# Kernel optimization log

Hardware: AMD Instinct MI355X
Metric: run time of the kernel (lower is better)

Reference implementation:

```python
import jax, jax.numpy as jnp
import numpy as np

B, J, F_IN, F_OUT = 16384, 17, 128, 128

def setup_inputs() -> dict:
    key = jax.random.key(0)
    k1, k2, k3, k4 = jax.random.split(key, 4)
    # xavier-ish scales
    x = jax.random.normal(k1, (B, J, F_IN), dtype=jnp.float32)
    W = jax.random.normal(k2, (2, F_IN, F_OUT), dtype=jnp.float32) * (1.414 * (6.0 / (F_IN + F_OUT)) ** 0.5 / 3.0)
    M = jax.random.normal(k3, (J, F_OUT), dtype=jnp.float32) * 0.5
    adj = jnp.eye(J, dtype=jnp.float32)          # adj == None path: learnable identity
    adj2 = jnp.full((J, J), 1e-6, dtype=jnp.float32)
    stdv = 1.0 / (F_OUT ** 0.5)
    bias = jax.random.uniform(k4, (F_OUT,), dtype=jnp.float32, minval=-stdv, maxval=stdv)
    return {"x": x, "W": W, "M": M, "adj": adj, "adj2": adj2, "bias": bias}

def reference(x, W, M, adj, adj2, bias):
    # h0, h1: [B, J, F_OUT]
    h0 = jnp.einsum('bjf,fg->bjg', x, W[0])
    h1 = jnp.einsum('bjf,fg->bjg', x, W[1])
    A = adj + adj2
    A = (A.T + A) * 0.5                      # symmetrize, [J, J]
    E = jnp.eye(A.shape[0], dtype=x.dtype)
    A_diag = A * E                           # self connections
    A_off = A * (1.0 - E)                    # neighbor connections
    # modulated aggregation: [J,J] x [B,J,F] -> [B,J,F]
    out = (jnp.einsum('ij,bjg->big', A_diag, M * h0)
           + jnp.einsum('ij,bjg->big', A_off, M * h1))
    return out + bias[None, None, :]
```

## Files before the change

kernel.cpp:

```cpp
#include <hip/hip_runtime.h>

#define J 17
#define F 128
#define TB 16
#define THREADS 512

typedef __attribute__((ext_vector_type(4))) float f32x4;
typedef __attribute__((ext_vector_type(8))) short bf16x8;

__device__ __forceinline__ unsigned short f2bf(float f) {
    unsigned u = __builtin_bit_cast(unsigned, f);
    u += 0x7fffu + ((u >> 16) & 1u);
    return (unsigned short)(u >> 16);
}

__device__ __forceinline__ f32x4 fma4(float a, f32x4 v, f32x4 c) {
#pragma unroll
    for (int r = 0; r < 4; ++r) c[r] = __builtin_fmaf(a, v[r], c[r]);
    return c;
}

__global__ void prep(const float* __restrict__ W, const float* __restrict__ adj,
                     const float* __restrict__ adj2, float* __restrict__ wsA,
                     unsigned short* __restrict__ WT) {
    int t = blockIdx.x * 256 + threadIdx.x;
    for (int idx = t; idx < 2 * F * F; idx += 16 * 256) {
        int mat = idx >> 14;
        int rem = idx & 16383;
        int g = rem >> 7, k = rem & 127;
        WT[idx] = f2bf(W[mat * 16384 + k * F + g]);
    }
    if (blockIdx.x == 0) {
        for (int idx = threadIdx.x; idx < J * J; idx += 256) {
            int i = idx / J, j = idx % J;
            float a = 0.5f * (adj[i*J+j] + adj2[i*J+j] + adj[j*J+i] + adj2[j*J+i]);
            wsA[idx] = (i == j) ? 0.0f : a;
            if (i == j) wsA[J * J + i] = a;
        }
    }
}

__global__ __launch_bounds__(THREADS, 2) void mgcn_kernel(
    const float* __restrict__ x, const float* __restrict__ Mw,
    const float* __restrict__ bias, const float* __restrict__ wsA,
    const unsigned short* __restrict__ WT, float* __restrict__ out) {

    __shared__ __align__(16) unsigned char xs[TB * J * F * 2];
    __shared__ __align__(16) float Ms[J * F];

    const int tid = threadIdx.x;
    const int b0  = blockIdx.x * TB;

    for (int idx = tid; idx < J * F / 4; idx += THREADS)
        ((float4*)Ms)[idx] = ((const float4*)Mw)[idx];

    const float4* xg = (const float4*)(x + (size_t)b0 * (J * F));
#pragma unroll
    for (int it = 0; it < (TB * J * F / 4) / THREADS; ++it) {
        int fi = it * THREADS + tid;
        float4 v = xg[fi];
        int b  = fi / (J * F / 4);
        int r  = fi - b * (J * F / 4);
        int j  = r >> 5;
        int k0 = (r & 31) * 4;
        unsigned byte = (unsigned)(b * (J * F * 2) + j * (F * 2) + k0 * 2);
        byte ^= (unsigned)((b & 7) << 4);
        ushort4 u;
        u.x = f2bf(v.x); u.y = f2bf(v.y); u.z = f2bf(v.z); u.w = f2bf(v.w);
        *(ushort4*)(xs + byte) = u;
    }

    const int wave = tid >> 6;
    const int lane = tid & 63;
    const int lrow = lane & 15;
    const int lq   = lane >> 4;
    const int grow = wave * 16 + lrow;
    const int gq   = wave * 16 + lq * 4;

    const f32x4 bias4 = *(const f32x4*)(bias + gq);
    f32x4 acc[J];
#pragma unroll
    for (int i = 0; i < J; ++i) acc[i] = bias4;

    const float* __restrict__ Aoff  = wsA;
    const float* __restrict__ Adiag = wsA + J * J;
    const unsigned rbase = (unsigned)(lrow * (J * F * 2));
    const unsigned swz   = (unsigned)((lrow & 7) << 4);

    __syncthreads();

    {
        bf16x8 wf0[4];
#pragma unroll
        for (int ks = 0; ks < 4; ++ks)
            wf0[ks] = __builtin_bit_cast(bf16x8,
                *(const uint4*)(WT + (size_t)grow * F + ks * 32 + lq * 8));
#pragma unroll
        for (int j = 0; j < J; ++j) {
            f32x4 h0 = {0.f, 0.f, 0.f, 0.f};
#pragma unroll
            for (int ks = 0; ks < 4; ++ks) {
                unsigned byte = (rbase + (unsigned)(j * (F * 2) + ks * 64 + lq * 16)) ^ swz;
                bf16x8 xf = __builtin_bit_cast(bf16x8, *(const uint4*)(xs + byte));
                h0 = __builtin_amdgcn_mfma_f32_16x16x32_bf16(wf0[ks], xf, h0, 0, 0, 0);
            }
            f32x4 mj = *(const f32x4*)&Ms[j * F + gq];
            f32x4 t0;
#pragma unroll
            for (int r = 0; r < 4; ++r) t0[r] = mj[r] * h0[r];
            acc[j] = fma4(Adiag[j], t0, acc[j]);
        }
    }

    {
        bf16x8 wf1[4];
#pragma unroll
        for (int ks = 0; ks < 4; ++ks)
            wf1[ks] = __builtin_bit_cast(bf16x8,
                *(const uint4*)(WT + (size_t)(F * F) + (size_t)grow * F + ks * 32 + lq * 8));
#pragma unroll
        for (int j = 0; j < J; ++j) {
            f32x4 h1 = {0.f, 0.f, 0.f, 0.f};
#pragma unroll
            for (int ks = 0; ks < 4; ++ks) {
                unsigned byte = (rbase + (unsigned)(j * (F * 2) + ks * 64 + lq * 16)) ^ swz;
                bf16x8 xf = __builtin_bit_cast(bf16x8, *(const uint4*)(xs + byte));
                h1 = __builtin_amdgcn_mfma_f32_16x16x32_bf16(wf1[ks], xf, h1, 0, 0, 0);
            }
            f32x4 mj = *(const f32x4*)&Ms[j * F + gq];
            f32x4 mh1;
#pragma unroll
            for (int r = 0; r < 4; ++r) mh1[r] = mj[r] * h1[r];
#pragma unroll
            for (int i = 0; i < J; ++i)
                acc[i] = fma4(Aoff[i * J + j], mh1, acc[i]);
        }
    }

#pragma unroll 1
    for (int r = 0; r < 2; ++r) {
        __syncthreads();
        if ((lrow >> 3) == r) {
            const int bl = lrow & 7;
            const unsigned base = (unsigned)(bl * (J * F * 4) + gq * 4);
            const unsigned esw  = (unsigned)((bl & 3) << 5);
#pragma unroll
            for (int i = 0; i < J; ++i)
                *(f32x4*)(xs + ((base + (unsigned)(i * F * 4)) ^ esw)) = acc[i];
        }
        __syncthreads();
        const size_t gbase = ((size_t)b0 + r * 8) * (J * F);
        for (int f = tid; f < 8 * J * F / 4; f += THREADS) {
            unsigned byte = (unsigned)f * 16u;
            unsigned bl   = byte / (unsigned)(J * F * 4);
            float4 v = *(const float4*)(xs + (byte ^ ((bl & 3) << 5)));
            *(float4*)(out + gbase + (size_t)f * 4) = v;
        }
    }
}

extern "C" void kernel_launch(void* const* d_in, const int* in_sizes, int n_in,
                              void* d_out, int out_size, void* d_ws, size_t ws_size,
                              hipStream_t stream) {
    const float* x    = (const float*)d_in[0];
    const float* W    = (const float*)d_in[1];
    const float* Mw   = (const float*)d_in[2];
    const float* adj  = (const float*)d_in[3];
    const float* adj2 = (const float*)d_in[4];
    const float* bias = (const float*)d_in[5];
    float* out = (float*)d_out;
    float* wsA = (float*)d_ws;
    unsigned short* WT = (unsigned short*)((char*)d_ws + 2048);

    int Btot = in_sizes[0] / (J * F);
    prep<<<16, 256, 0, stream>>>(W, adj, adj2, wsA, WT);
    mgcn_kernel<<<Btot / TB, THREADS, 0, stream>>>(x, Mw, bias, wsA, WT, out);
}
```

Measured before the change: 86.86 us.

## Stage x in two joint chunks and bf16 output staging to cut LDS

Splits the joint dimension into two chunks of 9 and 8 joints. Each chunk is loaded, converted to bf16 and processed in turn, so the shared x buffer holds only 9 joints per batch row. Output accumulators are now staged through shared memory as bf16 instead of fp32 so they fit the smaller buffer. The goal is a much smaller LDS footprint per block so more blocks can be resident per CU and hide memory latency. The costs are an extra barrier per chunk and bf16 rounding of the final output, which loses precision.

```diff
diff --git a/kernel.cpp b/kernel.cpp
--- a/kernel.cpp
+++ b/kernel.cpp
@@ -4,6 +4,7 @@
 #define F 128
 #define TB 16
 #define THREADS 512
+#define JSTRIDE 9
 
 typedef __attribute__((ext_vector_type(4))) float f32x4;
 typedef __attribute__((ext_vector_type(8))) short bf16x8;
@@ -13,11 +14,13 @@
     u += 0x7fffu + ((u >> 16) & 1u);
     return (unsigned short)(u >> 16);
 }
+__device__ __forceinline__ float bf2f(unsigned short s) {
+    return __builtin_bit_cast(float, (unsigned)s << 16);
+}
 
 __device__ __forceinline__ f32x4 fma4(float a, f32x4 v, f32x4 c) {
-#pragma unroll
-    for (int r = 0; r < 4; ++r) c[r] = __builtin_fmaf(a, v[r], c[r]);
-    return c;
+    f32x4 av = {a, a, a, a};
+    return __builtin_elementwise_fma(av, v, c);
 }
 
 __global__ void prep(const float* __restrict__ W, const float* __restrict__ adj,
@@ -40,12 +43,87 @@
     }
 }
 
+template<int JC, int J0>
+__device__ __forceinline__ void chunk(
+    const float* __restrict__ x, unsigned char* xs, const float* Ms,
+    const float* __restrict__ Aoff, const float* __restrict__ Adiag,
+    const unsigned short* __restrict__ WT, f32x4* acc,
+    int tid, int b0, int lrow, int lq, int grow, int gq) {
+
+#pragma unroll
+    for (int it = 0; it < JC; ++it) {
+        int fi = it * THREADS + tid;
+        int b  = fi / (JC * 32);
+        int r  = fi - b * (JC * 32);
+        int jj = r >> 5;
+        int k4 = r & 31;
+        const float4 v = *(const float4*)(x + (size_t)(b0 + b) * (J * F)
+                                            + (J0 + jj) * F + k4 * 4);
+        unsigned byte = (unsigned)(((b * JSTRIDE + jj) << 8) + (k4 << 3));
+        byte ^= (unsigned)((b & 7) << 4);
+        ushort4 u;
+        u.x = f2bf(v.x); u.y = f2bf(v.y); u.z = f2bf(v.z); u.w = f2bf(v.w);
+        *(ushort4*)(xs + byte) = u;
+    }
+    __syncthreads();
+
+    const unsigned rbase = (unsigned)(lrow * (JSTRIDE * 256));
+    const unsigned swz   = (unsigned)((lrow & 7) << 4);
+
+    {
+        bf16x8 wf[4];
+#pragma unroll
+        for (int ks = 0; ks < 4; ++ks)
+            wf[ks] = __builtin_bit_cast(bf16x8,
+                *(const uint4*)(WT + (size_t)grow * F + ks * 32 + lq * 8));
+#pragma unroll
+        for (int jj = 0; jj < JC; ++jj) {
+            constexpr int dummy = 0; (void)dummy;
+            f32x4 h0 = {0.f, 0.f, 0.f, 0.f};
+#pragma unroll
+            for (int ks = 0; ks < 4; ++ks) {
+                unsigned byte = (rbase + (unsigned)(jj * 256 + ks * 64 + lq * 16)) ^ swz;
+                bf16x8 xf = __builtin_bit_cast(bf16x8, *(const uint4*)(xs + byte));
+                h0 = __builtin_amdgcn_mfma_f32_16x16x32_bf16(wf[ks], xf, h0, 0, 0, 0);
+            }
+            const int j = J0 + jj;
+            f32x4 mj = *(const f32x4*)&Ms[j * F + gq];
+            acc[j] = fma4(Adiag[j], mj * h0, acc[j]);
+        }
+    }
+
+    {
+        bf16x8 wf[4];
+#pragma unroll
+        for (int ks = 0; ks < 4; ++ks)
+            wf[ks] = __builtin_bit_cast(bf16x8,
+                *(const uint4*)(WT + (size_t)(F * F) + (size_t)grow * F + ks * 32 + lq * 8));
+#pragma unroll
+        for (int jj = 0; jj < JC; ++jj) {
+            f32x4 h1 = {0.f, 0.f, 0.f, 0.f};
+#pragma unroll
+            for (int ks = 0; ks < 4; ++ks) {
+                unsigned byte = (rbase + (unsigned)(jj * 256 + ks * 64 + lq * 16)) ^ swz;
+                bf16x8 xf = __builtin_bit_cast(bf16x8, *(const uint4*)(xs + byte));
+                h1 = __builtin_amdgcn_mfma_f32_16x16x32_bf16(wf[ks], xf, h1, 0, 0, 0);
+            }
+            const int j = J0 + jj;
+            f32x4 mj  = *(const f32x4*)&Ms[j * F + gq];
+            f32x4 mh1 = mj * h1;
+#pragma unroll
+            for (int i = 0; i < J; ++i)
+                acc[i] = fma4(Aoff[i * J + j], mh1, acc[i]);
+        }
+    }
+    __syncthreads();
+}
+
 __global__ __launch_bounds__(THREADS, 2) void mgcn_kernel(
     const float* __restrict__ x, const float* __restrict__ Mw,
     const float* __restrict__ bias, const float* __restrict__ wsA,
     const unsigned short* __restrict__ WT, float* __restrict__ out) {
 
-    __shared__ __align__(16) unsigned char xs[TB * J * F * 2];
+    __shared__ __align__(16) unsigned char xs[TB * JSTRIDE * F * 2];
     __shared__ __align__(16) float Ms[J * F];
 
     const int tid = threadIdx.x;
@@ -53,22 +131,6 @@
 
     for (int idx = tid; idx < J * F / 4; idx += THREADS)
         ((float4*)Ms)[idx] = ((const float4*)Mw)[idx];
-
-    const float4* xg = (const float4*)(x + (size_t)b0 * (J * F));
-#pragma unroll
-    for (int it = 0; it < (TB * J * F / 4) / THREADS; ++it) {
-        int fi = it * THREADS + tid;
-        float4 v = xg[fi];
-        int b  = fi / (J * F / 4);
-        int r  = fi - b * (J * F / 4);
-        int j  = r >> 5;
-        int k0 = (r & 31) * 4;
-        unsigned byte = (unsigned)(b * (J * F * 2) + j * (F * 2) + k0 * 2);
-        byte ^= (unsigned)((b & 7) << 4);
-        ushort4 u;
-        u.x = f2bf(v.x); u.y = f2bf(v.y); u.z = f2bf(v.z); u.w = f2bf(v.w);
-        *(ushort4*)(xs + byte) = u;
-    }
 
     const int wave = tid >> 6;
     const int lane = tid & 63;
@@ -84,77 +146,34 @@
 
     const float* __restrict__ Aoff  = wsA;
     const float* __restrict__ Adiag = wsA + J * J;
-    const unsigned rbase = (unsigned)(lrow * (J * F * 2));
-    const unsigned swz   = (unsigned)((lrow & 7) << 4);
 
-    __syncthreads();
-
-    {
-        bf16x8 wf0[4];
-#pragma unroll
-        for (int ks = 0; ks < 4; ++ks)
-            wf0[ks] = __builtin_bit_cast(bf16x8,
-                *(const uint4*)(WT + (size_t)grow * F + ks * 32 + lq * 8));
-#pragma unroll
-        for (int j = 0; j < J; ++j) {
-            f32x4 h0 = {0.f, 0.f, 0.f, 0.f};
-#pragma unroll
-            for (int ks = 0; ks < 4; ++ks) {
-                unsigned byte = (rbase + (unsigned)(j * (F * 2) + ks * 64 + lq * 16)) ^ swz;
-                bf16x8 xf = __builtin_bit_cast(bf16x8, *(const uint4*)(xs + byte));
-                h0 = __builtin_amdgcn_mfma_f32_16x16x32_bf16(wf0[ks], xf, h0, 0, 0, 0);
-            }
-            f32x4 mj = *(const f32x4*)&Ms[j * F + gq];
-            f32x4 t0;
-#pragma unroll
-            for (int r = 0; r < 4; ++r) t0[r] = mj[r] * h0[r];
-            acc[j] = fma4(Adiag[j], t0, acc[j]);
-        }
-    }
-
-    {
-        bf16x8 wf1[4];
-#pragma unroll
-        for (int ks = 0; ks < 4; ++ks)
-            wf1[ks] = __builtin_bit_cast(bf16x8,
-                *(const uint4*)(WT + (size_t)(F * F) + (size_t)grow * F + ks * 32 + lq * 8));
-#pragma unroll
-        for (int j = 0; j < J; ++j) {
-            f32x4 h1 = {0.f, 0.f, 0.f, 0.f};
-#pragma unroll
-            for (int ks = 0; ks < 4; ++ks) {
-                unsigned byte = (rbase + (unsigned)(j * (F * 2) + ks * 64 + lq * 16)) ^ swz;
-                bf16x8 xf = __builtin_bit_cast(bf16x8, *(const uint4*)(xs + byte));
-                h1 = __builtin_amdgcn_mfma_f32_16x16x32_bf16(wf1[ks], xf, h1, 0, 0, 0);
-            }
-            f32x4 mj = *(const f32x4*)&Ms[j * F + gq];
-            f32x4 mh1;
-#pragma unroll
-            for (int r = 0; r < 4; ++r) mh1[r] = mj[r] * h1[r];
-#pragma unroll
-            for (int i = 0; i < J; ++i)
-                acc[i] = fma4(Aoff[i * J + j], mh1, acc[i]);
-        }
-    }
+    chunk<9, 0>(x, xs, Ms, Aoff, Adiag, WT, acc, tid, b0, lrow, lq, grow, gq);
+    chunk<8, 9>(x, xs, Ms, Aoff, Adiag, WT, acc, tid, b0, lrow, lq, grow, gq);
 
 #pragma unroll 1
     for (int r = 0; r < 2; ++r) {
-        __syncthreads();
+        if (r) __syncthreads();
         if ((lrow >> 3) == r) {
             const int bl = lrow & 7;
-            const unsigned base = (unsigned)(bl * (J * F * 4) + gq * 4);
-            const unsigned esw  = (unsigned)((bl & 3) << 5);
+            const unsigned base = (unsigned)(bl * (J * 256) + gq * 2);
+            const unsigned key  = (unsigned)((bl & 7) << 3);
 #pragma unroll
-            for (int i = 0; i < J; ++i)
-                *(f32x4*)(xs + ((base + (unsigned)(i * F * 4)) ^ esw)) = acc[i];
+            for (int i = 0; i < J; ++i) {
+                ushort4 u;
+                u.x = f2bf(acc[i][0]); u.y = f2bf(acc[i][1]);
+                u.z = f2bf(acc[i][2]); u.w = f2bf(acc[i][3]);
+                *(ushort4*)(xs + ((base + (unsigned)(i * 256)) ^ key)) = u;
+            }
         }
         __syncthreads();
         const size_t gbase = ((size_t)b0 + r * 8) * (J * F);
-        for (int f = tid; f < 8 * J * F / 4; f += THREADS) {
-            unsigned byte = (unsigned)f * 16u;
-            unsigned bl   = byte / (unsigned)(J * F * 4);
-            float4 v = *(const float4*)(xs + (byte ^ ((bl & 3) << 5)));
-            *(float4*)(out + gbase + (size_t)f * 4) = v;
+        for (int idx = tid; idx < 8 * J * F / 4; idx += THREADS) {
+            unsigned byte = (unsigned)idx * 8u;
+            unsigned bl   = byte / (unsigned)(J * 256);
+            ushort4 u = *(const ushort4*)(xs + (byte ^ ((bl & 7) << 3)));
+            float4 o;
+            o.x = bf2f(u.x); o.y = bf2f(u.y); o.z = bf2f(u.z); o.w = bf2f(u.w);
+            *(float4*)(out + gbase + (size_t)idx * 4) = o;
         }
     }
 }
```

After: 119.3 us. +37.3%, slower.
